# Kernel optimization log

Measured on AMD Instinct MI355X. Metric: run time of the kernel, lower is better.

Reference implementation:

```python
import jax, jax.numpy as jnp
import numpy as np

T_TEST, B, F, H, N_OUT = 8192, 8, 100, 512, 1


def setup_inputs() -> dict:
    key = jax.random.key(0)
    ks = jax.random.split(key, 7)
    s = 0.05  # keep generated-weight magnitudes in a realistic hypernetwork range
    return {
        "x_test": jax.random.normal(ks[0], (T_TEST, B, F), dtype=jnp.float32),
        "w1": jax.random.normal(ks[1], (B, F, H), dtype=jnp.float32) * s,
        "b1": jax.random.normal(ks[2], (B, H), dtype=jnp.float32) * s,
        "w2": jax.random.normal(ks[3], (B, H, H), dtype=jnp.float32) * s,
        "b2": jax.random.normal(ks[4], (B, H), dtype=jnp.float32) * s,
        "w3": jax.random.normal(ks[5], (B, H, N_OUT), dtype=jnp.float32) * s,
        "b3": jax.random.normal(ks[6], (B, N_OUT), dtype=jnp.float32) * s,
    }


def reference(x_test, w1, b1, w2, b2, w3, b3):
    # MotherNet.nn_forward with predicted_activation='relu',
    # weight_embedding_rank=None, low_rank_last=False.
    # Original torch: h = (x.unsqueeze(-1) * w.unsqueeze(0)).sum(2) + b
    # == per-dataset batched GEMM over the B axis.
    x = jnp.nan_to_num(x_test)                    # [T, B, F]
    h = jnp.einsum('tbf,bfh->tbh', x, w1) + b1    # [T, B, H]
    h = jax.nn.relu(h)
    h = jnp.einsum('tbf,bfh->tbh', h, w2) + b2    # [T, B, H]
    h = jax.nn.relu(h)
    h = jnp.einsum('tbf,bfh->tbh', h, w3) + b3    # [T, B, 1]
    return h
```

## Files before the change

kernel.cpp:

```cpp
#include <hip/hip_runtime.h>

#define T_TEST 8192
#define BB 8
#define FF 100
#define HH 512

typedef __bf16 bf16x8 __attribute__((ext_vector_type(8)));
typedef float f32x4 __attribute__((ext_vector_type(4)));
typedef unsigned short u16;
typedef unsigned int u32;

__device__ __forceinline__ u16 f2bf(float f) {
    u32 u = __float_as_uint(f);
    u += 0x7fffu + ((u >> 16) & 1);
    return (u16)(u >> 16);
}

__device__ __forceinline__ float nan2num(float v) {
    u32 u = __float_as_uint(v);
    if ((u & 0x7f800000u) == 0x7f800000u) {
        v = (u & 0x007fffffu) ? 0.f : ((u >> 31) ? -3.3895314e38f : 3.3895314e38f);
    }
    return v;
}

__global__ void prep_w1f(const float* __restrict__ w1, u16* __restrict__ w1f) {
    int tid = blockIdx.x * 256 + threadIdx.x;
    int lane = tid & 63;
    int kk = (tid >> 6) & 3;
    int n16 = (tid >> 8) & 31;
    int b = tid >> 13;
    int cc = lane & 15, qq = lane >> 4;
    int n = n16 * 16 + cc;
    u32 p[4];
#pragma unroll
    for (int jp = 0; jp < 4; ++jp) {
        int k0 = kk * 32 + qq * 8 + jp * 2;
        float v0 = (k0 < FF)     ? w1[(b * FF + k0) * HH + n]     : 0.f;
        float v1 = (k0 + 1 < FF) ? w1[(b * FF + k0 + 1) * HH + n] : 0.f;
        p[jp] = (u32)f2bf(v0) | ((u32)f2bf(v1) << 16);
    }
    uint4 o = {p[0], p[1], p[2], p[3]};
    size_t fi = ((size_t)(b * 4 + kk) * 32 + n16) * 64 + lane;
    *(uint4*)(w1f + fi * 8) = o;
}

__global__ void prep_w2f(const float* __restrict__ w2, u16* __restrict__ w2f) {
    int tid = blockIdx.x * 256 + threadIdx.x;
    int lane = tid & 63;
    int kk = (tid >> 6) & 15;
    int n16 = (tid >> 10) & 31;
    int b = tid >> 15;
    int cc = lane & 15, qq = lane >> 4;
    int n = n16 * 16 + cc;
    u32 p[4];
#pragma unroll
    for (int jp = 0; jp < 4; ++jp) {
        int k0 = kk * 32 + qq * 8 + jp * 2;
        float v0 = w2[(b * HH + k0) * HH + n];
        float v1 = w2[(b * HH + k0 + 1) * HH + n];
        p[jp] = (u32)f2bf(v0) | ((u32)f2bf(v1) << 16);
    }
    uint4 o = {p[0], p[1], p[2], p[3]};
    size_t fi = ((size_t)(b * 16 + kk) * 32 + n16) * 64 + lane;
    *(uint4*)(w2f + fi * 8) = o;
}

__device__ __forceinline__ int x_idx(int row, int k) {
    int g = k >> 3;
    int gp = (g & ~7) | ((g ^ row) & 7);
    return row * 128 + gp * 8 + (k & 7);
}
__device__ __forceinline__ int h1_idx(int row, int col) {
    int g = col >> 3;
    int gp = (g & ~7) | ((g ^ row) & 7);
    return row * 512 + gp * 8 + (col & 7);
}

__global__ __launch_bounds__(512, 4) void fused_mlp(
    const float* __restrict__ x, const u16* __restrict__ w1f,
    const float* __restrict__ b1, const u16* __restrict__ w2f,
    const float* __restrict__ b2, const float* __restrict__ w3,
    const float* __restrict__ b3, float* __restrict__ out) {
    __shared__ __align__(16) u16 h1_lds[64 * 512];
    __shared__ __align__(16) u16 x_lds[64 * 128];

    const int tid = threadIdx.x;
    const int b = blockIdx.x;
    const int m0 = blockIdx.y * 64;
    const int lane = tid & 63;
    const int w = tid >> 6;
    const int c = lane & 15, q = lane >> 4;
    const int n16b = w * 4;

    const bf16x8* W1 = (const bf16x8*)w1f + (size_t)b * 8192;
    const bf16x8* W2 = (const bf16x8*)w2f + (size_t)b * 32768;

    bf16x8 bc[4], bn[4];
#pragma unroll
    for (int ni = 0; ni < 4; ++ni)
        bc[ni] = W1[(0 * 32 + n16b + ni) * 64 + lane];

    {
        int row = tid >> 3, sub = tid & 7;
        const float* xr = x + ((size_t)(m0 + row) * BB + b) * FF;
        float4 v0 = *(const float4*)(xr + sub * 4);
        float4 v1 = *(const float4*)(xr + 32 + sub * 4);
        float4 v2 = *(const float4*)(xr + 64 + sub * 4);
        auto xw = [&](int k, float4 v) {
            ushort4 h;
            h.x = f2bf(nan2num(v.x));
            h.y = f2bf(nan2num(v.y));
            h.z = f2bf(nan2num(v.z));
            h.w = f2bf(nan2num(v.w));
            *(ushort4*)(&x_lds[x_idx(row, k)]) = h;
        };
        xw(sub * 4, v0);
        xw(32 + sub * 4, v1);
        xw(64 + sub * 4, v2);
        if (sub == 0) {
            float4 v3 = *(const float4*)(xr + 96);
            xw(96, v3);
            ushort4 z = {0, 0, 0, 0};
            *(ushort4*)(&x_lds[x_idx(row, 100)]) = z;
        } else if (sub <= 3) {
            int4 z = {0, 0, 0, 0};
            *(int4*)(&x_lds[x_idx(row, 96 + sub * 8)]) = z;
        }
    }
    __syncthreads();

    f32x4 acc1[4][4] = {};
#pragma unroll
    for (int kk = 0; kk < 4; ++kk) {
        if (kk < 3) {
#pragma unroll
            for (int ni = 0; ni < 4; ++ni)
                bn[ni] = W1[((kk + 1) * 32 + n16b + ni) * 64 + lane];
        }
        bf16x8 a[4];
#pragma unroll
        for (int mi = 0; mi < 4; ++mi)
            a[mi] = *(const bf16x8*)(&x_lds[x_idx(mi * 16 + c, (kk * 4 + q) * 8)]);
#pragma unroll
        for (int mi = 0; mi < 4; ++mi)
#pragma unroll
            for (int ni = 0; ni < 4; ++ni)
                acc1[mi][ni] = __builtin_amdgcn_mfma_f32_16x16x32_bf16(a[mi], bc[ni], acc1[mi][ni], 0, 0, 0);
        if (kk < 3) {
#pragma unroll
            for (int ni = 0; ni < 4; ++ni) bc[ni] = bn[ni];
        }
    }

#pragma unroll
    for (int ni = 0; ni < 4; ++ni)
        bc[ni] = W2[(0 * 32 + n16b + ni) * 64 + lane];

    {
        u32* h32 = (u32*)h1_lds;
        const float* b1g = b1 + b * HH;
#pragma unroll
        for (int ni = 0; ni < 4; ++ni) {
            int n = w * 64 + ni * 16 + c;
            float b1v = b1g[n];
            int ncol = n & ~1;
#pragma unroll
            for (int mi = 0; mi < 4; ++mi) {
                u32 own01 = (u32)f2bf(fmaxf(acc1[mi][ni][0] + b1v, 0.f)) |
                            ((u32)f2bf(fmaxf(acc1[mi][ni][1] + b1v, 0.f)) << 16);
                u32 own23 = (u32)f2bf(fmaxf(acc1[mi][ni][2] + b1v, 0.f)) |
                            ((u32)f2bf(fmaxf(acc1[mi][ni][3] + b1v, 0.f)) << 16);
                u32 oth01 = __shfl_xor(own01, 1, 64);
                u32 oth23 = __shfl_xor(own23, 1, 64);
                int row0 = mi * 16 + q * 4;
                if (!(c & 1)) {
                    u32 d0 = (own01 & 0xffffu) | (oth01 << 16);
                    u32 d1 = (own01 >> 16) | (oth01 & 0xffff0000u);
                    h32[h1_idx(row0, ncol) >> 1] = d0;
                    h32[h1_idx(row0 + 1, ncol) >> 1] = d1;
                } else {
                    u32 d2 = (oth23 & 0xffffu) | (own23 << 16);
                    u32 d3 = (oth23 >> 16) | (own23 & 0xffff0000u);
                    h32[h1_idx(row0 + 2, ncol) >> 1] = d2;
                    h32[h1_idx(row0 + 3, ncol) >> 1] = d3;
                }
            }
        }
    }
    __syncthreads();

    f32x4 acc2[4][4] = {};
#pragma unroll
    for (int kk = 0; kk < 16; ++kk) {
        if (kk < 15) {
#pragma unroll
            for (int ni = 0; ni < 4; ++ni)
                bn[ni] = W2[((kk + 1) * 32 + n16b + ni) * 64 + lane];
        }
        bf16x8 a[4];
#pragma unroll
        for (int mi = 0; mi < 4; ++mi)
            a[mi] = *(const bf16x8*)(&h1_lds[h1_idx(mi * 16 + c, (kk * 4 + q) * 8)]);
#pragma unroll
        for (int mi = 0; mi < 4; ++mi)
#pragma unroll
            for (int ni = 0; ni < 4; ++ni)
                acc2[mi][ni] = __builtin_amdgcn_mfma_f32_16x16x32_bf16(a[mi], bc[ni], acc2[mi][ni], 0, 0, 0);
        if (kk < 15) {
#pragma unroll
            for (int ni = 0; ni < 4; ++ni) bc[ni] = bn[ni];
        }
    }

    float ps[4][4] = {};
    {
        const float* b2g = b2 + b * HH;
        const float* w3g = w3 + b * HH;
#pragma unroll
        for (int ni = 0; ni < 4; ++ni) {
            int n = w * 64 + ni * 16 + c;
            float b2v = b2g[n];
            float w3v = w3g[n];
#pragma unroll
            for (int mi = 0; mi < 4; ++mi)
#pragma unroll
                for (int r = 0; r < 4; ++r)
                    ps[mi][r] += fmaxf(acc2[mi][ni][r] + b2v, 0.f) * w3v;
        }
    }
    float* part = (float*)x_lds;
#pragma unroll
    for (int mi = 0; mi < 4; ++mi)
#pragma unroll
        for (int r = 0; r < 4; ++r) {
            float v = ps[mi][r];
            v += __shfl_xor(v, 1, 64);
            v += __shfl_xor(v, 2, 64);
            v += __shfl_xor(v, 4, 64);
            v += __shfl_xor(v, 8, 64);
            if (c == 0) part[w * 64 + mi * 16 + q * 4 + r] = v;
        }
    __syncthreads();
    if (tid < 64) {
        float s = b3[b];
#pragma unroll
        for (int ww = 0; ww < 8; ++ww) s += part[ww * 64 + tid];
        out[(size_t)(m0 + tid) * BB + b] = s;
    }
}

extern "C" void kernel_launch(void* const* d_in, const int* in_sizes, int n_in,
                              void* d_out, int out_size, void* d_ws, size_t ws_size,
                              hipStream_t stream) {
    const float* x  = (const float*)d_in[0];
    const float* w1 = (const float*)d_in[1];
    const float* b1 = (const float*)d_in[2];
    const float* w2 = (const float*)d_in[3];
    const float* b2 = (const float*)d_in[4];
    const float* w3 = (const float*)d_in[5];
    const float* b3 = (const float*)d_in[6];
    float* out = (float*)d_out;

    u16* w1f = (u16*)d_ws;
    u16* w2f = w1f + (size_t)BB * 8192 * 8;

    prep_w1f<<<(BB * 4 * 32 * 64) / 256, 256, 0, stream>>>(w1, w1f);
    prep_w2f<<<(BB * 16 * 32 * 64) / 256, 256, 0, stream>>>(w2, w2f);

    fused_mlp<<<dim3(BB, T_TEST / 64), 512, 0, stream>>>(
        x, w1f, b1, w2f, b2, w3, b3, out);
}
```

Before: 144.9 us.

## Switch GEMMs to 32x32x16 MFMA tiles and merge weight-prep kernels

Replaces the 16x16x32 bf16 MFMA tiling with 32x32x16 MFMAs (2x2 tiles per wave), relays out the prepacked weight fragments to match, widens the LDS XOR swizzle to 16 groups, and double-buffers the weight fragment loads two k-steps ahead. The two weight-prep kernels are merged into one launch. The larger MFMA shape is meant to cut instruction count and register traffic for A/B operands per FLOP and to remove a launch. In exchange, the epilogue needs an extra shuffle stage and a changed row mapping, and the larger accumulators may affect register pressure.

```diff
diff --git a/kernel.cpp b/kernel.cpp
--- a/kernel.cpp
+++ b/kernel.cpp
@@ -6,7 +6,7 @@
 #define HH 512
 
 typedef __bf16 bf16x8 __attribute__((ext_vector_type(8)));
-typedef float f32x4 __attribute__((ext_vector_type(4)));
+typedef float f32x16 __attribute__((ext_vector_type(16)));
 typedef unsigned short u16;
 typedef unsigned int u32;
 
@@ -24,56 +24,56 @@
     return v;
 }
 
-__global__ void prep_w1f(const float* __restrict__ w1, u16* __restrict__ w1f) {
-    int tid = blockIdx.x * 256 + threadIdx.x;
-    int lane = tid & 63;
-    int kk = (tid >> 6) & 3;
-    int n16 = (tid >> 8) & 31;
-    int b = tid >> 13;
-    int cc = lane & 15, qq = lane >> 4;
-    int n = n16 * 16 + cc;
-    u32 p[4];
-#pragma unroll
-    for (int jp = 0; jp < 4; ++jp) {
-        int k0 = kk * 32 + qq * 8 + jp * 2;
-        float v0 = (k0 < FF)     ? w1[(b * FF + k0) * HH + n]     : 0.f;
-        float v1 = (k0 + 1 < FF) ? w1[(b * FF + k0 + 1) * HH + n] : 0.f;
-        p[jp] = (u32)f2bf(v0) | ((u32)f2bf(v1) << 16);
-    }
-    uint4 o = {p[0], p[1], p[2], p[3]};
-    size_t fi = ((size_t)(b * 4 + kk) * 32 + n16) * 64 + lane;
-    *(uint4*)(w1f + fi * 8) = o;
-}
-
-__global__ void prep_w2f(const float* __restrict__ w2, u16* __restrict__ w2f) {
-    int tid = blockIdx.x * 256 + threadIdx.x;
-    int lane = tid & 63;
-    int kk = (tid >> 6) & 15;
-    int n16 = (tid >> 10) & 31;
-    int b = tid >> 15;
-    int cc = lane & 15, qq = lane >> 4;
-    int n = n16 * 16 + cc;
-    u32 p[4];
-#pragma unroll
-    for (int jp = 0; jp < 4; ++jp) {
-        int k0 = kk * 32 + qq * 8 + jp * 2;
-        float v0 = w2[(b * HH + k0) * HH + n];
-        float v1 = w2[(b * HH + k0 + 1) * HH + n];
-        p[jp] = (u32)f2bf(v0) | ((u32)f2bf(v1) << 16);
-    }
-    uint4 o = {p[0], p[1], p[2], p[3]};
-    size_t fi = ((size_t)(b * 16 + kk) * 32 + n16) * 64 + lane;
-    *(uint4*)(w2f + fi * 8) = o;
+__global__ void prep_w(const float* __restrict__ w1, const float* __restrict__ w2,
+                       u16* __restrict__ w1f, u16* __restrict__ w2f) {
+    int bid = blockIdx.x;
+    if (bid < 256) {
+        int t = bid * 256 + threadIdx.x;
+        int lane = t & 63;
+        int n32 = (t >> 6) & 15;
+        int ks = (t >> 10) & 7;
+        int b = t >> 13;
+        int n = n32 * 32 + (lane & 31);
+        int kb = ks * 16 + (lane >> 5) * 8;
+        u32 p[4];
+#pragma unroll
+        for (int jp = 0; jp < 4; ++jp) {
+            int k0 = kb + jp * 2;
+            float v0 = (k0 < FF)     ? w1[(b * FF + k0) * HH + n]     : 0.f;
+            float v1 = (k0 + 1 < FF) ? w1[(b * FF + k0 + 1) * HH + n] : 0.f;
+            p[jp] = (u32)f2bf(v0) | ((u32)f2bf(v1) << 16);
+        }
+        uint4 o = {p[0], p[1], p[2], p[3]};
+        *(uint4*)(w1f + (size_t)t * 8) = o;
+    } else {
+        int t = (bid - 256) * 256 + threadIdx.x;
+        int lane = t & 63;
+        int n32 = (t >> 6) & 15;
+        int ks = (t >> 10) & 31;
+        int b = t >> 15;
+        int n = n32 * 32 + (lane & 31);
+        int kb = ks * 16 + (lane >> 5) * 8;
+        u32 p[4];
+#pragma unroll
+        for (int jp = 0; jp < 4; ++jp) {
+            int k0 = kb + jp * 2;
+            float v0 = w2[(b * HH + k0) * HH + n];
+            float v1 = w2[(b * HH + k0 + 1) * HH + n];
+            p[jp] = (u32)f2bf(v0) | ((u32)f2bf(v1) << 16);
+        }
+        uint4 o = {p[0], p[1], p[2], p[3]};
+        *(uint4*)(w2f + (size_t)t * 8) = o;
+    }
 }
 
 __device__ __forceinline__ int x_idx(int row, int k) {
     int g = k >> 3;
-    int gp = (g & ~7) | ((g ^ row) & 7);
+    int gp = g ^ (row & 15);
     return row * 128 + gp * 8 + (k & 7);
 }
 __device__ __forceinline__ int h1_idx(int row, int col) {
     int g = col >> 3;
-    int gp = (g & ~7) | ((g ^ row) & 7);
+    int gp = (g & ~15) | ((g ^ row) & 15);
     return row * 512 + gp * 8 + (col & 7);
 }
 
@@ -90,16 +90,17 @@
     const int m0 = blockIdx.y * 64;
     const int lane = tid & 63;
     const int w = tid >> 6;
-    const int c = lane & 15, q = lane >> 4;
-    const int n16b = w * 4;
-
-    const bf16x8* W1 = (const bf16x8*)w1f + (size_t)b * 8192;
-    const bf16x8* W2 = (const bf16x8*)w2f + (size_t)b * 32768;
-
-    bf16x8 bc[4], bn[4];
-#pragma unroll
-    for (int ni = 0; ni < 4; ++ni)
-        bc[ni] = W1[(0 * 32 + n16b + ni) * 64 + lane];
+    const int l31 = lane & 31, lh = lane >> 5;
+    const int n32b = w * 2;
+
+    const bf16x8* W1 = (const bf16x8*)w1f + (size_t)b * (8 * 16 * 64);
+    const bf16x8* W2 = (const bf16x8*)w2f + (size_t)b * (32 * 16 * 64);
+
+    bf16x8 bb[2][2];
+    bb[0][0] = W1[(0 * 16 + n32b + 0) * 64 + lane];
+    bb[0][1] = W1[(0 * 16 + n32b + 1) * 64 + lane];
+    bb[1][0] = W1[(1 * 16 + n32b + 0) * 64 + lane];
+    bb[1][1] = W1[(1 * 16 + n32b + 1) * 64 + lane];
 
     {
         int row = tid >> 3, sub = tid & 7;
@@ -130,116 +131,94 @@
     }
     __syncthreads();
 
-    f32x4 acc1[4][4] = {};
-#pragma unroll
-    for (int kk = 0; kk < 4; ++kk) {
-        if (kk < 3) {
-#pragma unroll
-            for (int ni = 0; ni < 4; ++ni)
-                bn[ni] = W1[((kk + 1) * 32 + n16b + ni) * 64 + lane];
-        }
-        bf16x8 a[4];
-#pragma unroll
-        for (int mi = 0; mi < 4; ++mi)
-            a[mi] = *(const bf16x8*)(&x_lds[x_idx(mi * 16 + c, (kk * 4 + q) * 8)]);
-#pragma unroll
-        for (int mi = 0; mi < 4; ++mi)
-#pragma unroll
-            for (int ni = 0; ni < 4; ++ni)
-                acc1[mi][ni] = __builtin_amdgcn_mfma_f32_16x16x32_bf16(a[mi], bc[ni], acc1[mi][ni], 0, 0, 0);
-        if (kk < 3) {
-#pragma unroll
-            for (int ni = 0; ni < 4; ++ni) bc[ni] = bn[ni];
-        }
-    }
-
-#pragma unroll
-    for (int ni = 0; ni < 4; ++ni)
-        bc[ni] = W2[(0 * 32 + n16b + ni) * 64 + lane];
+    f32x16 acc1[2][2] = {};
+#pragma unroll
+    for (int ks = 0; ks < 8; ++ks) {
+        bf16x8 a0 = *(const bf16x8*)(&x_lds[x_idx(l31,      (2 * ks + lh) * 8)]);
+        bf16x8 a1 = *(const bf16x8*)(&x_lds[x_idx(32 + l31, (2 * ks + lh) * 8)]);
+        acc1[0][0] = __builtin_amdgcn_mfma_f32_32x32x16_bf16(a0, bb[ks & 1][0], acc1[0][0], 0, 0, 0);
+        acc1[0][1] = __builtin_amdgcn_mfma_f32_32x32x16_bf16(a0, bb[ks & 1][1], acc1[0][1], 0, 0, 0);
+        acc1[1][0] = __builtin_amdgcn_mfma_f32_32x32x16_bf16(a1, bb[ks & 1][0], acc1[1][0], 0, 0, 0);
+        acc1[1][1] = __builtin_amdgcn_mfma_f32_32x32x16_bf16(a1, bb[ks & 1][1], acc1[1][1], 0, 0, 0);
+        if (ks < 6) {
+            bb[ks & 1][0] = W1[((ks + 2) * 16 + n32b + 0) * 64 + lane];
+            bb[ks & 1][1] = W1[((ks + 2) * 16 + n32b + 1) * 64 + lane];
+        }
+    }
+
+    bb[0][0] = W2[(0 * 16 + n32b + 0) * 64 + lane];
+    bb[0][1] = W2[(0 * 16 + n32b + 1) * 64 + lane];
+    bb[1][0] = W2[(1 * 16 + n32b + 0) * 64 + lane];
+    bb[1][1] = W2[(1 * 16 + n32b + 1) * 64 + lane];
 
     {
         u32* h32 = (u32*)h1_lds;
         const float* b1g = b1 + b * HH;
 #pragma unroll
-        for (int ni = 0; ni < 4; ++ni) {
-            int n = w * 64 + ni * 16 + c;
+        for (int ni = 0; ni < 2; ++ni) {
+            int n = (n32b + ni) * 32 + l31;
             float b1v = b1g[n];
             int ncol = n & ~1;
 #pragma unroll
-            for (int mi = 0; mi < 4; ++mi) {
-                u32 own01 = (u32)f2bf(fmaxf(acc1[mi][ni][0] + b1v, 0.f)) |
-                            ((u32)f2bf(fmaxf(acc1[mi][ni][1] + b1v, 0.f)) << 16);
-                u32 own23 = (u32)f2bf(fmaxf(acc1[mi][ni][2] + b1v, 0.f)) |
-                            ((u32)f2bf(fmaxf(acc1[mi][ni][3] + b1v, 0.f)) << 16);
-                u32 oth01 = __shfl_xor(own01, 1, 64);
-                u32 oth23 = __shfl_xor(own23, 1, 64);
-                int row0 = mi * 16 + q * 4;
-                if (!(c & 1)) {
-                    u32 d0 = (own01 & 0xffffu) | (oth01 << 16);
-                    u32 d1 = (own01 >> 16) | (oth01 & 0xffff0000u);
-                    h32[h1_idx(row0, ncol) >> 1] = d0;
-                    h32[h1_idx(row0 + 1, ncol) >> 1] = d1;
-                } else {
-                    u32 d2 = (oth23 & 0xffffu) | (own23 << 16);
-                    u32 d3 = (oth23 >> 16) | (own23 & 0xffff0000u);
-                    h32[h1_idx(row0 + 2, ncol) >> 1] = d2;
-                    h32[h1_idx(row0 + 3, ncol) >> 1] = d3;
+            for (int mi = 0; mi < 2; ++mi)
+#pragma unroll
+                for (int qd = 0; qd < 4; ++qd) {
+                    u32 own01 = (u32)f2bf(fmaxf(acc1[mi][ni][qd * 4 + 0] + b1v, 0.f)) |
+                                ((u32)f2bf(fmaxf(acc1[mi][ni][qd * 4 + 1] + b1v, 0.f)) << 16);
+                    u32 own23 = (u32)f2bf(fmaxf(acc1[mi][ni][qd * 4 + 2] + b1v, 0.f)) |
+                                ((u32)f2bf(fmaxf(acc1[mi][ni][qd * 4 + 3] + b1v, 0.f)) << 16);
+                    u32 oth01 = __shfl_xor(own01, 1, 64);
+                    u32 oth23 = __shfl_xor(own23, 1, 64);
+                    int row0 = mi * 32 + qd * 8 + lh * 4;
+                    if (!(lane & 1)) {
+                        u32 d0 = (own01 & 0xffffu) | (oth01 << 16);
+                        u32 d1 = (own01 >> 16) | (oth01 & 0xffff0000u);
+                        h32[h1_idx(row0, ncol) >> 1] = d0;
+                        h32[h1_idx(row0 + 1, ncol) >> 1] = d1;
+                    } else {
+                        u32 d2 = (oth23 & 0xffffu) | (own23 << 16);
+                        u32 d3 = (oth23 >> 16) | (own23 & 0xffff0000u);
+                        h32[h1_idx(row0 + 2, ncol) >> 1] = d2;
+                        h32[h1_idx(row0 + 3, ncol) >> 1] = d3;
+                    }
                 }
-            }
         }
     }
     __syncthreads();
 
-    f32x4 acc2[4][4] = {};
-#pragma unroll
-    for (int kk = 0; kk < 16; ++kk) {
-        if (kk < 15) {
-#pragma unroll
-            for (int ni = 0; ni < 4; ++ni)
-                bn[ni] = W2[((kk + 1) * 32 + n16b + ni) * 64 + lane];
-        }
-        bf16x8 a[4];
-#pragma unroll
-        for (int mi = 0; mi < 4; ++mi)
-            a[mi] = *(const bf16x8*)(&h1_lds[h1_idx(mi * 16 + c, (kk * 4 + q) * 8)]);
-#pragma unroll
-        for (int mi = 0; mi < 4; ++mi)
-#pragma unroll
-            for (int ni = 0; ni < 4; ++ni)
-                acc2[mi][ni] = __builtin_amdgcn_mfma_f32_16x16x32_bf16(a[mi], bc[ni], acc2[mi][ni], 0, 0, 0);
-        if (kk < 15) {
-#pragma unroll
-            for (int ni = 0; ni < 4; ++ni) bc[ni] = bn[ni];
-        }
-    }
-
-    float ps[4][4] = {};
-    {
-        const float* b2g = b2 + b * HH;
-        const float* w3g = w3 + b * HH;
-#pragma unroll
-        for (int ni = 0; ni < 4; ++ni) {
-            int n = w * 64 + ni * 16 + c;
-            float b2v = b2g[n];
-            float w3v = w3g[n];
-#pragma unroll
-            for (int mi = 0; mi < 4; ++mi)
-#pragma unroll
-                for (int r = 0; r < 4; ++r)
-                    ps[mi][r] += fmaxf(acc2[mi][ni][r] + b2v, 0.f) * w3v;
-        }
-    }
+    f32x16 acc2[2][2] = {};
+#pragma unroll
+    for (int ks = 0; ks < 32; ++ks) {
+        bf16x8 a0 = *(const bf16x8*)(&h1_lds[h1_idx(l31,      (2 * ks + lh) * 8)]);
+        bf16x8 a1 = *(const bf16x8*)(&h1_lds[h1_idx(32 + l31, (2 * ks + lh) * 8)]);
+        acc2[0][0] = __builtin_amdgcn_mfma_f32_32x32x16_bf16(a0, bb[ks & 1][0], acc2[0][0], 0, 0, 0);
+        acc2[0][1] = __builtin_amdgcn_mfma_f32_32x32x16_bf16(a0, bb[ks & 1][1], acc2[0][1], 0, 0, 0);
+        acc2[1][0] = __builtin_amdgcn_mfma_f32_32x32x16_bf16(a1, bb[ks & 1][0], acc2[1][0], 0, 0, 0);
+        acc2[1][1] = __builtin_amdgcn_mfma_f32_32x32x16_bf16(a1, bb[ks & 1][1], acc2[1][1], 0, 0, 0);
+        if (ks < 30) {
+            bb[ks & 1][0] = W2[((ks + 2) * 16 + n32b + 0) * 64 + lane];
+            bb[ks & 1][1] = W2[((ks + 2) * 16 + n32b + 1) * 64 + lane];
+        }
+    }
+
+    const float* b2g = b2 + b * HH;
+    const float* w3g = w3 + b * HH;
+    float b2v0 = b2g[(n32b + 0) * 32 + l31], w3v0 = w3g[(n32b + 0) * 32 + l31];
+    float b2v1 = b2g[(n32b + 1) * 32 + l31], w3v1 = w3g[(n32b + 1) * 32 + l31];
     float* part = (float*)x_lds;
 #pragma unroll
-    for (int mi = 0; mi < 4; ++mi)
-#pragma unroll
-        for (int r = 0; r < 4; ++r) {
-            float v = ps[mi][r];
+    for (int mi = 0; mi < 2; ++mi)
+#pragma unroll
+        for (int r = 0; r < 16; ++r) {
+            float v = fmaxf(acc2[mi][0][r] + b2v0, 0.f) * w3v0 +
+                      fmaxf(acc2[mi][1][r] + b2v1, 0.f) * w3v1;
             v += __shfl_xor(v, 1, 64);
             v += __shfl_xor(v, 2, 64);
             v += __shfl_xor(v, 4, 64);
             v += __shfl_xor(v, 8, 64);
-            if (c == 0) part[w * 64 + mi * 16 + q * 4 + r] = v;
+            v += __shfl_xor(v, 16, 64);
+            if (l31 == 0)
+                part[w * 64 + mi * 32 + (r & 3) + 8 * (r >> 2) + 4 * lh] = v;
         }
     __syncthreads();
     if (tid < 64) {
@@ -265,8 +244,7 @@
     u16* w1f = (u16*)d_ws;
     u16* w2f = w1f + (size_t)BB * 8192 * 8;
 
-    prep_w1f<<<(BB * 4 * 32 * 64) / 256, 256, 0, stream>>>(w1, w1f);
-    prep_w2f<<<(BB * 16 * 32 * 64) / 256, 256, 0, stream>>>(w2, w2f);
+    prep_w<<<1280, 256, 0, stream>>>(w1, w2, w1f, w2f);
 
     fused_mlp<<<dim3(BB, T_TEST / 64), 512, 0, stream>>>(
         x, w1f, b1, w2f, b2, w3, b3, out);
```

Result: faster. 137.3 us (-5.2%).
